# Optimization experiments

Hardware: AMD Instinct MI355X
Metric: run time of the kernel (lower is better)

## Reference

```python
import jax, jax.numpy as jnp
import numpy as np

B, N, D, H, C = 32, 128, 5000, 256, 4  # trees, nodes/tree, input_size_rumor, hidden, rumor_classes


def setup_inputs() -> dict:
    key = jax.random.key(0)
    ks = jax.random.split(key, 24)
    scale = 0.05  # xavier-like scale (module calls init_weight with xavier_uniform_)
    inp = {"x": jax.random.normal(ks[0], (B, N, D), dtype=jnp.float32)}
    names = ["Er", "Wsr_r", "Usr_r", "Wsr_z", "Usr_z", "Wsr_h", "Usr_h",
             "Wr_r", "Ur_r", "Usr2r_r", "Wr_z", "Ur_z", "Usr2r_z",
             "Wr_h", "Ur_h", "Usr2r_h"]
    shapes = [(H, D)] + [(H, H)] * 15
    for i, (n, s) in enumerate(zip(names, shapes)):
        inp[n] = jax.random.normal(ks[i + 1], s, dtype=jnp.float32) * scale
    inp["Vr"] = jax.random.normal(ks[17], (C, H), dtype=jnp.float32) * scale
    inp["br"] = jnp.zeros((C, 1), dtype=jnp.float32)
    # Tree structure: nodes in topological order; slot 0 = zero initial state,
    # node j is stored at slot j+1, parents[:, i] is the SLOT of node i's parent.
    rng = np.random.default_rng(0)
    pslot = np.zeros((B, N), dtype=np.int64)  # root's parent slot = 0 (zeros)
    for i in range(1, N):
        pslot[:, i] = rng.integers(1, i + 1, size=B)  # parent is an earlier node
    has_child = np.zeros((B, N), dtype=bool)
    for i in range(1, N):
        has_child[np.arange(B), pslot[:, i] - 1] = True
    inp["parents"] = jnp.asarray(pslot)
    inp["is_leaf"] = jnp.asarray(~has_child)
    return inp


def _tree_gru(x_tilde, parents, Wsr_r, Usr_r, Wsr_z, Usr_z, Wsr_h, Usr_h,
              Wr_r, Ur_r, Usr2r_r, Wr_z, Ur_z, Usr2r_z, Wr_h, Ur_h, Usr2r_h):
    """x_tilde: [B,N,H] embedded node features; parents: [B,N] parent SLOT ids.
    Returns h_rumor for every node: [B,N,H]. Same math as MultiModel.rumor_forward,
    with the Python recursion replaced by a scan over topologically-ordered nodes,
    vectorized across the batch of trees."""
    Bq, Nq, Hq = x_tilde.shape
    S0 = jnp.zeros((Bq, Nq + 1, Hq), x_tilde.dtype)  # slot 0 = initial zero state

    def step(carry, xs):
        S_sh, S_ru = carry  # [B, N+1, H] stored shared/rumor states
        xt, p, i = xs       # xt: [B,H], p: [B] parent slot, i: node index
        idx = p[:, None, None]
        hsp = jnp.take_along_axis(S_sh, idx, axis=1)[:, 0]  # [B,H] parent shared state
        hrp = jnp.take_along_axis(S_ru, idx, axis=1)[:, 0]  # [B,H] parent rumor state
        # shared GRU cell
        r_sh = jax.nn.sigmoid(xt @ Wsr_r.T + hsp @ Usr_r.T)
        z_sh = jax.nn.sigmoid(xt @ Wsr_z.T + hsp @ Usr_z.T)
        h_sh_t = jnp.tanh(xt @ Wsr_h.T + (hsp * r_sh) @ Usr_h.T)
        h_sh = (1 - z_sh) * hsp + z_sh * h_sh_t
        # rumor GRU cell (conditioned on shared state)
        r_ru = jax.nn.sigmoid(xt @ Wr_r.T + hrp @ Ur_r.T + h_sh @ Usr2r_r.T)
        z_ru = jax.nn.sigmoid(xt @ Wr_z.T + hrp @ Ur_z.T + h_sh @ Usr2r_z.T)
        h_ru_t = jnp.tanh(xt @ Wr_h.T + (hrp * r_ru) @ Ur_h.T + h_sh @ Usr2r_h.T)
        h_ru = (1 - z_ru) * hrp + z_ru * h_ru_t
        S_sh = S_sh.at[:, i + 1, :].set(h_sh)
        S_ru = S_ru.at[:, i + 1, :].set(h_ru)
        return (S_sh, S_ru), None

    xs = (jnp.swapaxes(x_tilde, 0, 1), parents.T, jnp.arange(Nq))
    (S_sh, S_ru), _ = jax.lax.scan(step, (S0, S0), xs)
    return S_ru[:, 1:, :]


def reference(x, Er, Wsr_r, Usr_r, Wsr_z, Usr_z, Wsr_h, Usr_h,
              Wr_r, Ur_r, Usr2r_r, Wr_z, Ur_z, Usr2r_z, Wr_h, Ur_h, Usr2r_h,
              Vr, br, parents, is_leaf):
    x_tilde = jnp.einsum('bnd,hd->bnh', x, Er)  # Er @ x for every node
    H_ru = _tree_gru(x_tilde, parents, Wsr_r, Usr_r, Wsr_z, Usr_z, Wsr_h, Usr_h,
                     Wr_r, Ur_r, Usr2r_r, Wr_z, Ur_z, Usr2r_z, Wr_h, Ur_h, Usr2r_h)
    # max over leaf node hidden vectors (torch.max over cat of leaf vectors)
    neg = jnp.finfo(H_ru.dtype).min
    hmax = jnp.where(is_leaf[:, :, None], H_ru, neg).max(axis=1)  # [B,H]
    logits = hmax @ Vr.T + br[:, 0]  # [B,C]
    return jax.nn.softmax(logits, axis=-1)
```

## Files before the change

### kernel.cpp

```cpp
#include <hip/hip_runtime.h>
#include <hip/hip_bf16.h>
#include <math.h>


#define H_DIM 256
#define N_NODES 128
#define B_TREES 32
#define MAXL 128
#define TPB 2
#define GRID_WGS 256

typedef short bf16x8 __attribute__((ext_vector_type(8)));
typedef float f32x4 __attribute__((ext_vector_type(4)));

__device__ __forceinline__ float sigmoidf_(float x) {
    return 1.0f / (1.0f + expf(-x));
}
__device__ __forceinline__ unsigned bfp(float x) {
    unsigned u = __float_as_uint(x);
    return (u + 0x7fffu + ((u >> 16) & 1u)) >> 16;
}
__device__ __forceinline__ float bflo(unsigned w) { return __uint_as_float(w << 16); }
__device__ __forceinline__ float bfhi(unsigned w) { return __uint_as_float(w & 0xffff0000u); }

__device__ __forceinline__ void unpack8(uint4 v, float* f) {
    f[0] = bflo(v.x); f[1] = bfhi(v.x);
    f[2] = bflo(v.y); f[3] = bfhi(v.y);
    f[4] = bflo(v.z); f[5] = bfhi(v.z);
    f[6] = bflo(v.w); f[7] = bfhi(v.w);
}

__device__ __forceinline__ float coh_load(const float* p) {
    return __hip_atomic_load(p, __ATOMIC_RELAXED, __HIP_MEMORY_SCOPE_AGENT);
}
__device__ __forceinline__ void coh_store(float* p, float v) {
    __hip_atomic_store(p, v, __ATOMIC_RELAXED, __HIP_MEMORY_SCOPE_AGENT);
}
__device__ __forceinline__ unsigned coh_loadu(const unsigned* p) {
    return __hip_atomic_load(p, __ATOMIC_RELAXED, __HIP_MEMORY_SCOPE_AGENT);
}
__device__ __forceinline__ void coh_storeu(unsigned* p, unsigned v) {
    __hip_atomic_store(p, v, __ATOMIC_RELAXED, __HIP_MEMORY_SCOPE_AGENT);
}

__global__ __launch_bounds__(256) void gemm_mfma_nt(
    const float* __restrict__ A, const float* __restrict__ B,
    float* __restrict__ C, int K, int ldc, int Kc, int zStride) {
    __shared__ short As[64][40];
    __shared__ short Bs[64][40];
    const int tid = threadIdx.x;
    const int bm = blockIdx.x, bn = blockIdx.y;
    const int z = blockIdx.z;
    const int k_begin = z * Kc;
    const int k_end = (k_begin + Kc < K) ? (k_begin + Kc) : K;
    float* Cz = C + (size_t)z * zStride;
    const int row = tid >> 2;
    const int quad = tid & 3;
    const int wave = tid >> 6;
    const int lane = tid & 63;
    const int lm = lane & 15;
    const int kq = lane >> 4;

    f32x4 acc[4];
#pragma unroll
    for (int i = 0; i < 4; ++i) acc[i] = (f32x4){0.f, 0.f, 0.f, 0.f};

    for (int k0 = k_begin; k0 < k_end; k0 += 32) {
        const int kbase = k0 + quad * 8;
        {
            float a8[8];
            const float* Ap = A + (size_t)(bm * 64 + row) * K + kbase;
            if (kbase + 8 <= k_end) {
                const float4 v0 = *(const float4*)Ap;
                const float4 v1 = *(const float4*)(Ap + 4);
                a8[0] = v0.x; a8[1] = v0.y; a8[2] = v0.z; a8[3] = v0.w;
                a8[4] = v1.x; a8[5] = v1.y; a8[6] = v1.z; a8[7] = v1.w;
            } else {
#pragma unroll
                for (int i = 0; i < 8; ++i)
                    a8[i] = (kbase + i < k_end) ? Ap[i] : 0.f;
            }
            uint4 v;
            v.x = bfp(a8[0]) | (bfp(a8[1]) << 16);
            v.y = bfp(a8[2]) | (bfp(a8[3]) << 16);
            v.z = bfp(a8[4]) | (bfp(a8[5]) << 16);
            v.w = bfp(a8[6]) | (bfp(a8[7]) << 16);
            *(uint4*)&As[row][quad * 8] = v;
        }
        {
            float b8[8];
            const float* Bp = B + (size_t)(bn * 64 + row) * K + kbase;
            if (kbase + 8 <= k_end) {
                const float4 v0 = *(const float4*)Bp;
                const float4 v1 = *(const float4*)(Bp + 4);
                b8[0] = v0.x; b8[1] = v0.y; b8[2] = v0.z; b8[3] = v0.w;
                b8[4] = v1.x; b8[5] = v1.y; b8[6] = v1.z; b8[7] = v1.w;
            } else {
#pragma unroll
                for (int i = 0; i < 8; ++i)
                    b8[i] = (kbase + i < k_end) ? Bp[i] : 0.f;
            }
            uint4 v;
            v.x = bfp(b8[0]) | (bfp(b8[1]) << 16);
            v.y = bfp(b8[2]) | (bfp(b8[3]) << 16);
            v.z = bfp(b8[4]) | (bfp(b8[5]) << 16);
            v.w = bfp(b8[6]) | (bfp(b8[7]) << 16);
            *(uint4*)&Bs[row][quad * 8] = v;
        }
        __syncthreads();
        const bf16x8 af = *(const bf16x8*)&As[wave * 16 + lm][kq * 8];
#pragma unroll
        for (int nt = 0; nt < 4; ++nt) {
            const bf16x8 bf = *(const bf16x8*)&Bs[nt * 16 + lm][kq * 8];
            acc[nt] = __builtin_amdgcn_mfma_f32_16x16x32_bf16(af, bf, acc[nt], 0, 0, 0);
        }
        __syncthreads();
    }
#pragma unroll
    for (int nt = 0; nt < 4; ++nt) {
#pragma unroll
        for (int r = 0; r < 4; ++r) {
            const int gm = bm * 64 + wave * 16 + kq * 4 + r;
            const int gn = bn * 64 + nt * 16 + lm;
            Cz[(size_t)gm * ldc + gn] = acc[nt][r];
        }
    }
}

__global__ __launch_bounds__(256) void reduce4_k(
    const float* __restrict__ Pp, float* __restrict__ xt) {
    const int i = (blockIdx.x * 256 + threadIdx.x) * 4;
    const float4 a = *(const float4*)(Pp + i);
    const float4 b = *(const float4*)(Pp + 1048576 + i);
    const float4 c = *(const float4*)(Pp + 2097152 + i);
    const float4 d = *(const float4*)(Pp + 3145728 + i);
    float4 s;
    s.x = a.x + b.x + c.x + d.x;
    s.y = a.y + b.y + c.y + d.y;
    s.z = a.z + b.z + c.z + d.z;
    s.w = a.w + b.w + c.w + d.w;
    *(float4*)(xt + i) = s;
}

__global__ __launch_bounds__(256) void transpose_pack_u(
    const float* __restrict__ U0, const float* __restrict__ U1,
    const float* __restrict__ U2, const float* __restrict__ U3,
    const float* __restrict__ U4, const float* __restrict__ U5,
    const float* __restrict__ U6, const float* __restrict__ U7,
    const float* __restrict__ U8, uint4* __restrict__ UTb) {
    const float* Us[9] = {U0, U1, U2, U3, U4, U5, U6, U7, U8};
    const int jb = blockIdx.x;
    const int m = blockIdx.y;
    const int h = threadIdx.x;
    const float* U = Us[m] + (size_t)h * 256 + jb * 8;
    uint4 v;
    v.x = bfp(U[0]) | (bfp(U[1]) << 16);
    v.y = bfp(U[2]) | (bfp(U[3]) << 16);
    v.z = bfp(U[4]) | (bfp(U[5]) << 16);
    v.w = bfp(U[6]) | (bfp(U[7]) << 16);
    UTb[(size_t)(m * 32 + jb) * 256 + h] = v;
}

__global__ __launch_bounds__(256) void build_schedule(
    const int* __restrict__ parents, int* __restrict__ sched,
    int* __restrict__ level_off, int* __restrict__ gstart,
    int* __restrict__ gend, int* __restrict__ ngrp,
    unsigned* __restrict__ ready) {
    __shared__ unsigned char depth[B_TREES][N_NODES];
    __shared__ int counts[MAXL];
    __shared__ int base[MAXL + 1];
    const int tid = threadIdx.x;
    for (int k = tid; k < B_TREES * N_NODES; k += 256)
        coh_storeu(&ready[k], 0u);
    for (int k = tid; k < MAXL; k += 256) counts[k] = 0;
    __syncthreads();
    if (tid < B_TREES) {
        depth[tid][0] = 0;
        for (int i = 1; i < N_NODES; ++i) {
            const int p = parents[tid * N_NODES + i];
            depth[tid][i] = (unsigned char)(depth[tid][p - 1] + 1);
        }
    }
    __syncthreads();
    for (int k = tid; k < B_TREES * N_NODES; k += 256)
        atomicAdd(&counts[depth[k >> 7][k & 127]], 1);
    __syncthreads();
    if (tid == 0) {
        int acc = 0;
        int nl = 0;
        for (int l = 0; l < MAXL; ++l) {
            base[l] = acc;
            acc += counts[l];
            if (counts[l] > 0) nl = l + 1;
        }
        base[MAXL] = acc;
        level_off[MAXL + 1] = nl;
        int ng = 0;
        for (int l = 0; l < nl; ++l) {
            for (int s = base[l]; s < base[l + 1]; s += TPB) {
                gstart[ng] = s;
                gend[ng] = (s + TPB < base[l + 1]) ? s + TPB : base[l + 1];
                ++ng;
            }
        }
        *ngrp = ng;
    }
    __syncthreads();
    for (int k = tid; k <= MAXL; k += 256) level_off[k] = base[k];
    for (int k = tid; k < MAXL; k += 256) counts[k] = 0;
    __syncthreads();
    for (int k = tid; k < B_TREES * N_NODES; k += 256) {
        const int d = depth[k >> 7][k & 127];
        const int pos = base[d] + atomicAdd(&counts[d], 1);
        sched[pos] = k;
    }
}

__global__ __launch_bounds__(256, 1) void tree_scan_df(
    const float* __restrict__ P, const uint4* __restrict__ UTb,
    const int* __restrict__ parents,
    const int* __restrict__ sched,
    const int* __restrict__ gstart, const int* __restrict__ gend,
    const int* __restrict__ ngrp, unsigned* __restrict__ ready,
    float* __restrict__ Ssh, float* __restrict__ Sru) {
    const int h = threadIdx.x;
    const int wg = blockIdx.x;
    __shared__ float hsp_s[H_DIM][TPB];
    __shared__ float hrp_s[H_DIM][TPB];
    __shared__ float aux_s[H_DIM][TPB];
    __shared__ float hsh_s[H_DIM][TPB];

    const uint4* __restrict__ U0b = UTb + 0 * 8192;
    const uint4* __restrict__ U1b = UTb + 1 * 8192;
    const uint4* __restrict__ U2b = UTb + 2 * 8192;
    const uint4* __restrict__ U3b = UTb + 3 * 8192;
    const uint4* __restrict__ U4b = UTb + 4 * 8192;
    const uint4* __restrict__ U5b = UTb + 5 * 8192;
    const uint4* __restrict__ U6b = UTb + 6 * 8192;
    const uint4* __restrict__ U7b = UTb + 7 * 8192;
    const uint4* __restrict__ U8b = UTb + 8 * 8192;

    const int ng = ngrp[0];
    for (int g = wg; g < ng; g += GRID_WGS) {
        const int s = gstart[g];
        const int e = gend[g];
        if (h < e - s) {
            const int nd = sched[s + h];
            const int p = parents[nd];
            if (p != 0) {
                const unsigned* f = &ready[(nd & ~127) + p - 1];
                while (coh_loadu(f) == 0u) __builtin_amdgcn_s_sleep(1);
            }
        }
        __syncthreads();

        int  node[TPB];
        bool val[TPB];
        float phs[TPB], phr[TPB];
#pragma unroll
        for (int t = 0; t < TPB; ++t) {
            const int idx = s + t;
            val[t] = idx < e;
            const int nd = val[t] ? sched[idx] : sched[s];
            node[t] = nd;
            const int p = parents[nd];
            float hs = 0.f, hr = 0.f;
            if (p != 0) {
                const size_t pr = ((size_t)((nd & ~127) + p - 1)) * H_DIM + h;
                hs = coh_load(&Ssh[pr]);
                hr = coh_load(&Sru[pr]);
            }
            phs[t] = hs;
            phr[t] = hr;
        }
        *(float2*)&hsp_s[h][0] = make_float2(phs[0], phs[1]);
        *(float2*)&hrp_s[h][0] = make_float2(phr[0], phr[1]);
        __syncthreads();

        float pr_[TPB], pz_[TPB];
#pragma unroll
        for (int t = 0; t < TPB; ++t) {
            const float* Pi = P + (size_t)node[t] * 1536;
            pr_[t] = Pi[h];
            pz_[t] = Pi[256 + h];
        }
        float dr[TPB] = {0.f, 0.f};
        float dz[TPB] = {0.f, 0.f};
#pragma unroll 4
        for (int jb = 0; jb < 32; ++jb) {
            const uint4 w0 = U0b[jb * 256 + h];
            const uint4 w1 = U1b[jb * 256 + h];
            float a[8], c[8];
            unpack8(w0, a);
            unpack8(w1, c);
#pragma unroll
            for (int q = 0; q < 8; ++q) {
                const float2 hv = *(const float2*)&hsp_s[jb * 8 + q][0];
                dr[0] = fmaf(a[q], hv.x, dr[0]);
                dr[1] = fmaf(a[q], hv.y, dr[1]);
                dz[0] = fmaf(c[q], hv.x, dz[0]);
                dz[1] = fmaf(c[q], hv.y, dz[1]);
            }
        }
        float z_sh[TPB], vsh[TPB];
#pragma unroll
        for (int t = 0; t < TPB; ++t) {
            const float r_sh = sigmoidf_(pr_[t] + dr[t]);
            z_sh[t] = sigmoidf_(pz_[t] + dz[t]);
            vsh[t] = phs[t] * r_sh;
        }
        *(float2*)&aux_s[h][0] = make_float2(vsh[0], vsh[1]);
        __syncthreads();

        float ph_[TPB];
#pragma unroll
        for (int t = 0; t < TPB; ++t)
            ph_[t] = P[(size_t)node[t] * 1536 + 512 + h];
        float dh[TPB] = {0.f, 0.f};
#pragma unroll 8
        for (int jb = 0; jb < 32; ++jb) {
            const uint4 w2 = U2b[jb * 256 + h];
            float a[8];
            unpack8(w2, a);
#pragma unroll
            for (int q = 0; q < 8; ++q) {
                const float2 hv = *(const float2*)&aux_s[jb * 8 + q][0];
                dh[0] = fmaf(a[q], hv.x, dh[0]);
                dh[1] = fmaf(a[q], hv.y, dh[1]);
            }
        }
        float hsh[TPB];
#pragma unroll
        for (int t = 0; t < TPB; ++t) {
            const float hsh_t = tanhf(ph_[t] + dh[t]);
            hsh[t] = (1.f - z_sh[t]) * phs[t] + z_sh[t] * hsh_t;
            if (val[t])
                coh_store(&Ssh[(size_t)node[t] * H_DIM + h], hsh[t]);
        }
        *(float2*)&hsh_s[h][0] = make_float2(hsh[0], hsh[1]);
        __syncthreads();

        float pru_[TPB], pzu_[TPB];
#pragma unroll
        for (int t = 0; t < TPB; ++t) {
            const float* Pi = P + (size_t)node[t] * 1536;
            pru_[t] = Pi[768 + h];
            pzu_[t] = Pi[1024 + h];
        }
        float er[TPB] = {0.f, 0.f};
        float ez[TPB] = {0.f, 0.f};
        float fr[TPB] = {0.f, 0.f};
        float fz[TPB] = {0.f, 0.f};
#pragma unroll 2
        for (int jb = 0; jb < 32; ++jb) {
            const uint4 w3 = U3b[jb * 256 + h];
            const uint4 w4 = U4b[jb * 256 + h];
            const uint4 w6 = U6b[jb * 256 + h];
            const uint4 w7 = U7b[jb * 256 + h];
            float a3[8], a4[8], a6[8], a7[8];
            unpack8(w3, a3);
            unpack8(w4, a4);
            unpack8(w6, a6);
            unpack8(w7, a7);
#pragma unroll
            for (int q = 0; q < 8; ++q) {
                const float2 hr2 = *(const float2*)&hrp_s[jb * 8 + q][0];
                const float2 hs2 = *(const float2*)&hsh_s[jb * 8 + q][0];
                er[0] = fmaf(a3[q], hr2.x, er[0]);
                er[1] = fmaf(a3[q], hr2.y, er[1]);
                ez[0] = fmaf(a4[q], hr2.x, ez[0]);
                ez[1] = fmaf(a4[q], hr2.y, ez[1]);
                fr[0] = fmaf(a6[q], hs2.x, fr[0]);
                fr[1] = fmaf(a6[q], hs2.y, fr[1]);
                fz[0] = fmaf(a7[q], hs2.x, fz[0]);
                fz[1] = fmaf(a7[q], hs2.y, fz[1]);
            }
        }
        float z_ru[TPB], v2[TPB];
#pragma unroll
        for (int t = 0; t < TPB; ++t) {
            const float r_ru = sigmoidf_(pru_[t] + er[t] + fr[t]);
            z_ru[t] = sigmoidf_(pzu_[t] + ez[t] + fz[t]);
            v2[t] = phr[t] * r_ru;
        }
        *(float2*)&aux_s[h][0] = make_float2(v2[0], v2[1]);
        __syncthreads();

        float phu_[TPB];
#pragma unroll
        for (int t = 0; t < TPB; ++t)
            phu_[t] = P[(size_t)node[t] * 1536 + 1280 + h];
        float eh[TPB] = {0.f, 0.f};
        float fh[TPB] = {0.f, 0.f};
#pragma unroll 4
        for (int jb = 0; jb < 32; ++jb) {
            const uint4 w5 = U5b[jb * 256 + h];
            const uint4 w8 = U8b[jb * 256 + h];
            float a5[8], a8[8];
            unpack8(w5, a5);
            unpack8(w8, a8);
#pragma unroll
            for (int q = 0; q < 8; ++q) {
                const float2 v4 = *(const float2*)&aux_s[jb * 8 + q][0];
                const float2 s4 = *(const float2*)&hsh_s[jb * 8 + q][0];
                eh[0] = fmaf(a5[q], v4.x, eh[0]);
                eh[1] = fmaf(a5[q], v4.y, eh[1]);
                fh[0] = fmaf(a8[q], s4.x, fh[0]);
                fh[1] = fmaf(a8[q], s4.y, fh[1]);
            }
        }
#pragma unroll
        for (int t = 0; t < TPB; ++t) {
            const float hru_t = tanhf(phu_[t] + eh[t] + fh[t]);
            const float h_ru = (1.f - z_ru[t]) * phr[t] + z_ru[t] * hru_t;
            if (val[t])
                coh_store(&Sru[(size_t)node[t] * H_DIM + h], h_ru);
        }
        __syncthreads();
        if (h < e - s)
            coh_storeu(&ready[sched[s + h]], 1u);
        __syncthreads();
    }
}

__global__ __launch_bounds__(256) void epilogue_k(
    const float* __restrict__ Sru, const int* __restrict__ is_leaf,
    const float* __restrict__ Vr, const float* __restrict__ br,
    float* __restrict__ out) {
    const int b = blockIdx.x;
    const int h = threadIdx.x;
    float m = -3.402823466e38f;
    for (int n = 0; n < N_NODES; ++n) {
        const float v = Sru[((size_t)b * N_NODES + n) * H_DIM + h];
        if (is_leaf[b * N_NODES + n] != 0) m = fmaxf(m, v);
    }
    __shared__ float hm[H_DIM];
    __shared__ float lg[4];
    hm[h] = m;
    __syncthreads();
    if (h < 4) {
        float acc = br[h];
#pragma unroll 8
        for (int j = 0; j < H_DIM; ++j) acc = fmaf(Vr[h * 256 + j], hm[j], acc);
        lg[h] = acc;
    }
    __syncthreads();
    if (h == 0) {
        const float mx = fmaxf(fmaxf(lg[0], lg[1]), fmaxf(lg[2], lg[3]));
        const float e0 = expf(lg[0] - mx);
        const float e1 = expf(lg[1] - mx);
        const float e2 = expf(lg[2] - mx);
        const float e3 = expf(lg[3] - mx);
        const float s = e0 + e1 + e2 + e3;
        out[b * 4 + 0] = e0 / s;
        out[b * 4 + 1] = e1 / s;
        out[b * 4 + 2] = e2 / s;
        out[b * 4 + 3] = e3 / s;
    }
}

extern "C" void kernel_launch(void* const* d_in, const int* in_sizes, int n_in,
                              void* d_out, int out_size, void* d_ws, size_t ws_size,
                              hipStream_t stream) {
    const float* x      = (const float*)d_in[0];
    const float* Er     = (const float*)d_in[1];
    const float* Wsr_r  = (const float*)d_in[2];
    const float* Usr_r  = (const float*)d_in[3];
    const float* Wsr_z  = (const float*)d_in[4];
    const float* Usr_z  = (const float*)d_in[5];
    const float* Wsr_h  = (const float*)d_in[6];
    const float* Usr_h  = (const float*)d_in[7];
    const float* Wr_r   = (const float*)d_in[8];
    const float* Ur_r   = (const float*)d_in[9];
    const float* Usr2r_r= (const float*)d_in[10];
    const float* Wr_z   = (const float*)d_in[11];
    const float* Ur_z   = (const float*)d_in[12];
    const float* Usr2r_z= (const float*)d_in[13];
    const float* Wr_h   = (const float*)d_in[14];
    const float* Ur_h   = (const float*)d_in[15];
    const float* Usr2r_h= (const float*)d_in[16];
    const float* Vr     = (const float*)d_in[17];
    const float* br     = (const float*)d_in[18];
    const int*   parents= (const int*)d_in[19];
    const int*   is_leaf= (const int*)d_in[20];
    float* out = (float*)d_out;

    float* ws = (float*)d_ws;
    float* xt   = ws;
    float* P    = xt + 1048576;
    float* Wcat = P + 6291456;
    uint4* UTb  = (uint4*)(Wcat + 393216);
    float* Ssh  = (float*)(UTb + 73728);
    float* Sru  = Ssh + 1048576;
    int*   sched     = (int*)(Sru + 1048576);
    int*   level_off = sched + 4096;
    unsigned* ready  = (unsigned*)(level_off + 192);
    int*   gstart    = (int*)(ready + 4096);
    int*   gend      = gstart + 4096;
    int*   ngrp      = gend + 4096;

    dim3 blk(256);

    gemm_mfma_nt<<<dim3(64, 4, 4), blk, 0, stream>>>(x, Er, P, 5000, 256,
                                                     1280, 1048576);
    reduce4_k<<<dim3(1024), blk, 0, stream>>>(P, xt);

    const float* Ws6[6] = {Wsr_r, Wsr_z, Wsr_h, Wr_r, Wr_z, Wr_h};
    for (int w = 0; w < 6; ++w)
        (void)hipMemcpyAsync(Wcat + (size_t)w * 65536, Ws6[w],
                             65536 * sizeof(float), hipMemcpyDeviceToDevice,
                             stream);
    gemm_mfma_nt<<<dim3(64, 24, 1), blk, 0, stream>>>(xt, Wcat, P, 256, 1536,
                                                      256, 0);

    transpose_pack_u<<<dim3(32, 9), blk, 0, stream>>>(
        Usr_r, Usr_z, Usr_h, Ur_r, Ur_z, Ur_h, Usr2r_r, Usr2r_z, Usr2r_h, UTb);

    build_schedule<<<dim3(1), blk, 0, stream>>>(parents, sched, level_off,
                                                gstart, gend, ngrp, ready);

    void* args[] = {(void*)&P, (void*)&UTb, (void*)&parents, (void*)&sched,
                    (void*)&gstart, (void*)&gend, (void*)&ngrp, (void*)&ready,
                    (void*)&Ssh, (void*)&Sru};
    (void)hipLaunchCooperativeKernel((const void*)tree_scan_df,
                                     dim3(GRID_WGS), blk, args, 0, stream);

    epilogue_k<<<dim3(B_TREES), blk, 0, stream>>>(Sru, is_leaf, Vr, br, out);
}
```

Baseline: 822.5 us.

## Use atomic ticket for dynamic group scheduling and drop weight concat copies

The tree scan kernel now has each workgroup claim the next node group from a global atomic ticket counter instead of taking groups in a fixed stride by block index, which should cut stalls caused by imbalanced dependency waits. A new GEMM variant reads the six input-weight matrices directly through per-tile pointer selection, which removes six device-to-device memcpys into a concatenated buffer. The ticket adds one atomic and one barrier per group, and the memcpy removal saves several small launches.

```diff
diff --git a/kernel.cpp b/kernel.cpp
--- a/kernel.cpp
+++ b/kernel.cpp
@@ -127,6 +127,73 @@
     }
 }
 
+__global__ __launch_bounds__(256) void gemm_mfma_w6(
+    const float* __restrict__ A,
+    const float* __restrict__ B0, const float* __restrict__ B1,
+    const float* __restrict__ B2, const float* __restrict__ B3,
+    const float* __restrict__ B4, const float* __restrict__ B5,
+    float* __restrict__ C, int ldc) {
+    __shared__ short As[64][40];
+    __shared__ short Bs[64][40];
+    const int tid = threadIdx.x;
+    const int bm = blockIdx.x, bn = blockIdx.y;
+    const float* Bsel[6] = {B0, B1, B2, B3, B4, B5};
+    const int row = tid >> 2;
+    const int quad = tid & 3;
+    const int wave = tid >> 6;
+    const int lane = tid & 63;
+    const int lm = lane & 15;
+    const int kq = lane >> 4;
+    const float* Brow = Bsel[bn >> 2] + (size_t)((bn & 3) * 64 + row) * 256;
+    const float* Arow = A + (size_t)(bm * 64 + row) * 256;
+
+    f32x4 acc[4];
+#pragma unroll
+    for (int i = 0; i < 4; ++i) acc[i] = (f32x4){0.f, 0.f, 0.f, 0.f};
+
+#pragma unroll
+    for (int kt = 0; kt < 8; ++kt) {
+        const int kbase = kt * 32 + quad * 8;
+        {
+            const float4 v0 = *(const float4*)(Arow + kbase);
+            const float4 v1 = *(const float4*)(Arow + kbase + 4);
+            uint4 v;
+            v.x = bfp(v0.x) | (bfp(v0.y) << 16);
+            v.y = bfp(v0.z) | (bfp(v0.w) << 16);
+            v.z = bfp(v1.x) | (bfp(v1.y) << 16);
+            v.w = bfp(v1.z) | (bfp(v1.w) << 16);
+            *(uint4*)&As[row][quad * 8] = v;
+        }
+        {
+            const float4 v0 = *(const float4*)(Brow + kbase);
+            const float4 v1 = *(const float4*)(Brow + kbase + 4);
+            uint4 v;
+            v.x = bfp(v0.x) | (bfp(v0.y) << 16);
+            v.y = bfp(v0.z) | (bfp(v0.w) << 16);
+            v.z = bfp(v1.x) | (bfp(v1.y) << 16);
+            v.w = bfp(v1.z) | (bfp(v1.w) << 16);
+            *(uint4*)&Bs[row][quad * 8] = v;
+        }
+        __syncthreads();
+        const bf16x8 af = *(const bf16x8*)&As[wave * 16 + lm][kq * 8];
+#pragma unroll
+        for (int nt = 0; nt < 4; ++nt) {
+            const bf16x8 bf = *(const bf16x8*)&Bs[nt * 16 + lm][kq * 8];
+            acc[nt] = __builtin_amdgcn_mfma_f32_16x16x32_bf16(af, bf, acc[nt], 0, 0, 0);
+        }
+        __syncthreads();
+    }
+#pragma unroll
+    for (int nt = 0; nt < 4; ++nt) {
+#pragma unroll
+        for (int r = 0; r < 4; ++r) {
+            const int gm = bm * 64 + wave * 16 + kq * 4 + r;
+            const int gn = bn * 64 + nt * 16 + lm;
+            C[(size_t)gm * ldc + gn] = acc[nt][r];
+        }
+    }
+}
+
 __global__ __launch_bounds__(256) void reduce4_k(
     const float* __restrict__ Pp, float* __restrict__ xt) {
     const int i = (blockIdx.x * 256 + threadIdx.x) * 4;
@@ -165,11 +232,12 @@
     const int* __restrict__ parents, int* __restrict__ sched,
     int* __restrict__ level_off, int* __restrict__ gstart,
     int* __restrict__ gend, int* __restrict__ ngrp,
-    unsigned* __restrict__ ready) {
+    unsigned* __restrict__ ready, unsigned* __restrict__ ticket) {
     __shared__ unsigned char depth[B_TREES][N_NODES];
     __shared__ int counts[MAXL];
     __shared__ int base[MAXL + 1];
     const int tid = threadIdx.x;
+    if (tid == 0) coh_storeu(ticket, 0u);
     for (int k = tid; k < B_TREES * N_NODES; k += 256)
         coh_storeu(&ready[k], 0u);
     for (int k = tid; k < MAXL; k += 256) counts[k] = 0;
@@ -222,13 +290,14 @@
     const int* __restrict__ sched,
     const int* __restrict__ gstart, const int* __restrict__ gend,
     const int* __restrict__ ngrp, unsigned* __restrict__ ready,
+    unsigned* __restrict__ ticket,
     float* __restrict__ Ssh, float* __restrict__ Sru) {
     const int h = threadIdx.x;
-    const int wg = blockIdx.x;
     __shared__ float hsp_s[H_DIM][TPB];
     __shared__ float hrp_s[H_DIM][TPB];
     __shared__ float aux_s[H_DIM][TPB];
     __shared__ float hsh_s[H_DIM][TPB];
+    __shared__ int g_sh;
 
     const uint4* __restrict__ U0b = UTb + 0 * 8192;
     const uint4* __restrict__ U1b = UTb + 1 * 8192;
@@ -241,7 +310,11 @@
     const uint4* __restrict__ U8b = UTb + 8 * 8192;
 
     const int ng = ngrp[0];
-    for (int g = wg; g < ng; g += GRID_WGS) {
+    for (;;) {
+        if (h == 0) g_sh = (int)atomicAdd(ticket, 1u);
+        __syncthreads();
+        const int g = g_sh;
+        if (g >= ng) break;
         const int s = gstart[g];
         const int e = gend[g];
         if (h < e - s) {
@@ -498,6 +571,7 @@
     int*   gstart    = (int*)(ready + 4096);
     int*   gend      = gstart + 4096;
     int*   ngrp      = gend + 4096;
+    unsigned* ticket = (unsigned*)(ngrp + 16);
 
     dim3 blk(256);
 
@@ -505,23 +579,19 @@
                                                      1280, 1048576);
     reduce4_k<<<dim3(1024), blk, 0, stream>>>(P, xt);
 
-    const float* Ws6[6] = {Wsr_r, Wsr_z, Wsr_h, Wr_r, Wr_z, Wr_h};
-    for (int w = 0; w < 6; ++w)
-        (void)hipMemcpyAsync(Wcat + (size_t)w * 65536, Ws6[w],
-                             65536 * sizeof(float), hipMemcpyDeviceToDevice,
-                             stream);
-    gemm_mfma_nt<<<dim3(64, 24, 1), blk, 0, stream>>>(xt, Wcat, P, 256, 1536,
-                                                      256, 0);
+    gemm_mfma_w6<<<dim3(64, 24), blk, 0, stream>>>(
+        xt, Wsr_r, Wsr_z, Wsr_h, Wr_r, Wr_z, Wr_h, P, 1536);
 
     transpose_pack_u<<<dim3(32, 9), blk, 0, stream>>>(
         Usr_r, Usr_z, Usr_h, Ur_r, Ur_z, Ur_h, Usr2r_r, Usr2r_z, Usr2r_h, UTb);
 
     build_schedule<<<dim3(1), blk, 0, stream>>>(parents, sched, level_off,
-                                                gstart, gend, ngrp, ready);
+                                                gstart, gend, ngrp, ready,
+                                                ticket);
 
     void* args[] = {(void*)&P, (void*)&UTb, (void*)&parents, (void*)&sched,
                     (void*)&gstart, (void*)&gend, (void*)&ngrp, (void*)&ready,
-                    (void*)&Ssh, (void*)&Sru};
+                    (void*)&ticket, (void*)&Ssh, (void*)&Sru};
     (void)hipLaunchCooperativeKernel((const void*)tree_scan_df,
                                      dim3(GRID_WGS), blk, args, 0, stream);
 
```

After: 828.6 us. About the same (+0.7%).
